# Kernel optimization log

Hardware: AMD Instinct MI355X
Metric: run time of the kernel (lower is better)

The kernel has to match this reference:

```python
import jax, jax.numpy as jnp
import numpy as np

B, C, H, W = 16, 512, 32, 32
COND_C, L_COND = 768, 77
N_GROUPS, N_HEADS = 8, 8
HEAD = C // N_HEADS
EPS = 1e-5


def setup_inputs() -> dict:
    key = jax.random.key(0)
    ks = jax.random.split(key, 6)
    s = lambda fan_in: 1.0 / np.sqrt(fan_in)
    return {
        "x_0": jax.random.normal(ks[0], (B, C, H, W), jnp.float32),
        "cond": jax.random.normal(ks[1], (B, L_COND, COND_C), jnp.float32),
        "gn_gamma": jnp.ones((C,), jnp.float32),
        "gn_beta": jnp.zeros((C,), jnp.float32),
        "qkv_w": jax.random.normal(ks[2], (3 * C, C), jnp.float32) * s(C),
        "qkv_b": jnp.zeros((3 * C,), jnp.float32),
        "cond_kv_w": jax.random.normal(ks[3], (2 * C, COND_C), jnp.float32) * s(COND_C),
        "cond_kv_b": jnp.zeros((2 * C,), jnp.float32),
        "out_w": jax.random.normal(ks[4], (C, C), jnp.float32) * s(C),
        "out_b": jnp.zeros((C,), jnp.float32),
    }


def reference(x_0, cond, gn_gamma, gn_beta, qkv_w, qkv_b, cond_kv_w, cond_kv_b, out_w, out_b):
    b, c, h, w = x_0.shape
    L = h * w
    # --- GroupNorm over (C/G, H, W) per group, per-channel affine ---
    xg = x_0.reshape(b, N_GROUPS, c // N_GROUPS, h * w)
    mu = xg.mean(axis=(2, 3), keepdims=True)
    var = xg.var(axis=(2, 3), keepdims=True)
    xn = ((xg - mu) * jax.lax.rsqrt(var + EPS)).reshape(b, c, h, w)
    xn = xn * gn_gamma[None, :, None, None] + gn_beta[None, :, None, None]
    # --- to tokens [B, L, C] ---
    x = xn.transpose(0, 2, 3, 1).reshape(b, L, c)
    # --- QKV ---
    qkv = x @ qkv_w.T + qkv_b  # [B, L, 3C]
    q, k, v = jnp.split(qkv, 3, axis=-1)
    q = q.reshape(b, L, N_HEADS, HEAD)
    k = k.reshape(b, L, N_HEADS, HEAD)
    v = v.reshape(b, L, N_HEADS, HEAD)
    # --- conditional K/V ---
    kv_c = cond @ cond_kv_w.T + cond_kv_b  # [B, Lc, 2C]
    k_c, v_c = jnp.split(kv_c, 2, axis=-1)
    Lc = cond.shape[1]
    k_c = k_c.reshape(b, Lc, N_HEADS, HEAD)
    v_c = v_c.reshape(b, Lc, N_HEADS, HEAD)
    K = jnp.concatenate([k, k_c], axis=1)  # [B, L+Lc, H, D]
    V = jnp.concatenate([v, v_c], axis=1)
    # --- attention (full score matrix, as in the original) ---
    scale = HEAD ** -0.5
    scores = jnp.einsum("bqhd,bkhd->bhqk", q, K) * scale
    att = jax.nn.softmax(scores, axis=-1)
    out = jnp.einsum("bhqk,bkhd->bqhd", att, V).reshape(b, L, c)
    out = out @ out_w.T + out_b
    # --- back to image + residual ---
    out = out.reshape(b, h, w, c).transpose(0, 3, 1, 2)
    return out + x_0
```

## Files before the change

### kernel.cpp

```cpp
#include <hip/hip_runtime.h>

typedef short bf16x8 __attribute__((ext_vector_type(8)));
typedef float f32x4 __attribute__((ext_vector_type(4)));
typedef float f32x16 __attribute__((ext_vector_type(16)));
typedef unsigned int u32x4 __attribute__((ext_vector_type(4)));

#define KVP 1152

__device__ __forceinline__ unsigned short f2b(float f) {
    unsigned int u = __float_as_uint(f);
    u += 0x7FFFu + ((u >> 16) & 1u);
    return (unsigned short)(u >> 16);
}

__device__ __forceinline__ f32x4 mfma16(bf16x8 a, bf16x8 b, f32x4 c) {
    return __builtin_amdgcn_mfma_f32_16x16x32_bf16(a, b, c, 0, 0, 0);
}
__device__ __forceinline__ f32x16 mfma32(bf16x8 a, bf16x8 b, f32x16 c) {
    return __builtin_amdgcn_mfma_f32_32x32x16_bf16(a, b, c, 0, 0, 0);
}
__device__ __forceinline__ float exp2_raw(float x) {
    float r; asm("v_exp_f32 %0, %1" : "=v"(r) : "v"(x)); return r;
}
__device__ __forceinline__ unsigned cvt_pk(float lo, float hi) {
    unsigned r; asm("v_cvt_pk_bf16_f32 %0, %1, %2" : "=v"(r) : "v"(lo), "v"(hi)); return r;
}

typedef __attribute__((address_space(3))) unsigned int lds_u32_t;
typedef const __attribute__((address_space(1))) unsigned int glb_u32_t;
__device__ __forceinline__ void async_cp16(const void* g, void* l) {
    __builtin_amdgcn_global_load_lds((glb_u32_t*)(unsigned long long)g,
                                     (lds_u32_t*)(unsigned int)(unsigned long long)l,
                                     16, 0, 0);
}

__global__ __launch_bounds__(256) void gn_stats_k(const float* __restrict__ x, float* __restrict__ stats) {
    int bg = blockIdx.x;
    const float4* p = (const float4*)(x + (size_t)bg * 64 * 1024);
    float s = 0.f, ss = 0.f;
    for (int i = threadIdx.x; i < 16384; i += 256) {
        float4 v = p[i];
        s  += v.x + v.y + v.z + v.w;
        ss += v.x * v.x + v.y * v.y + v.z * v.z + v.w * v.w;
    }
#pragma unroll
    for (int o = 32; o; o >>= 1) { s += __shfl_down(s, o); ss += __shfl_down(ss, o); }
    __shared__ float red[8];
    int w = threadIdx.x >> 6;
    if ((threadIdx.x & 63) == 0) { red[w] = s; red[4 + w] = ss; }
    __syncthreads();
    if (threadIdx.x == 0) {
        s  = red[0] + red[1] + red[2] + red[3];
        ss = red[4] + red[5] + red[6] + red[7];
        float mean = s * (1.f / 65536.f);
        float var  = ss * (1.f / 65536.f) - mean * mean;
        stats[2 * bg]     = mean;
        stats[2 * bg + 1] = rsqrtf(var + 1e-5f);
    }
}

__global__ __launch_bounds__(256) void gn_apply_k(const float* __restrict__ x, const float* __restrict__ stats,
                                                  const float* __restrict__ gamma, const float* __restrict__ beta,
                                                  unsigned short* __restrict__ xt) {
    int st = blockIdx.x & 15;
    int ct = (blockIdx.x >> 4) & 7;
    int b  = blockIdx.x >> 7;
    float mean = stats[2 * (b * 8 + ct)];
    float rsig = stats[2 * (b * 8 + ct) + 1];
    __shared__ unsigned short tile[64][65];
    int tid = threadIdx.x;
#pragma unroll
    for (int it = 0; it < 4; ++it) {
        int idx = it * 256 + tid;
        int ci = idx >> 4, j4 = idx & 15;
        int c = ct * 64 + ci;
        float4 v = *(const float4*)(x + ((size_t)b * 512 + c) * 1024 + st * 64 + j4 * 4);
        float gs = gamma[c] * rsig;
        float bo = beta[c] - mean * gs;
        tile[j4 * 4 + 0][ci] = f2b(v.x * gs + bo);
        tile[j4 * 4 + 1][ci] = f2b(v.y * gs + bo);
        tile[j4 * 4 + 2][ci] = f2b(v.z * gs + bo);
        tile[j4 * 4 + 3][ci] = f2b(v.w * gs + bo);
    }
    __syncthreads();
#pragma unroll
    for (int it = 0; it < 4; ++it) {
        int idx = it * 256 + tid;
        int si = idx >> 4, q = idx & 15;
        uint2 u;
        u.x = (unsigned)tile[si][q * 4 + 0] | ((unsigned)tile[si][q * 4 + 1] << 16);
        u.y = (unsigned)tile[si][q * 4 + 2] | ((unsigned)tile[si][q * 4 + 3] << 16);
        *(uint2*)(xt + ((size_t)b * 1024 + st * 64 + si) * 512 + ct * 64 + q * 4) = u;
    }
}

__global__ __launch_bounds__(256) void cvt_k(const float* __restrict__ in, unsigned short* __restrict__ out, int n4) {
    int i = blockIdx.x * 256 + threadIdx.x;
    if (i < n4) {
        float4 v = ((const float4*)in)[i];
        uint2 u;
        u.x = (unsigned)f2b(v.x) | ((unsigned)f2b(v.y) << 16);
        u.y = (unsigned)f2b(v.z) | ((unsigned)f2b(v.w) << 16);
        ((uint2*)out)[i] = u;
    }
}

template <int EPI>
__global__ __launch_bounds__(256) void gemm128_k(const unsigned short* __restrict__ A,
                                                 const unsigned short* __restrict__ Bw,
                                                 const float* __restrict__ bias,
                                                 int M, int N, int K,
                                                 unsigned short* __restrict__ Qo,
                                                 unsigned short* __restrict__ Ko,
                                                 unsigned short* __restrict__ Vo,
                                                 const float* __restrict__ x0,
                                                 float* __restrict__ outp) {
    __shared__ __align__(16) unsigned short As[3][4096];
    __shared__ __align__(16) unsigned short Bs[3][4096];
    const int m0 = blockIdx.x * 128, n0 = blockIdx.y * 128;
    const int tid = threadIdx.x, lane = tid & 63, w = tid >> 6;
    const int wr = w >> 1, wc = w & 1;
    const int lc = lane & 15, lg = lane >> 4;

    const int sRow = lane >> 2;
    const int sSlot = (lane & 3) ^ ((lane >> 3) & 3);
    const unsigned short* aSrc0 = A + (size_t)(m0 + 16 * w + sRow) * K + sSlot * 8;
    const unsigned short* aSrc1 = A + (size_t)(m0 + 64 + 16 * w + sRow) * K + sSlot * 8;
    const unsigned short* bSrc0 = Bw + (size_t)(n0 + 16 * w + sRow) * K + sSlot * 8;
    const unsigned short* bSrc1 = Bw + (size_t)(n0 + 64 + 16 * w + sRow) * K + sSlot * 8;

    const int rSlot8 = (lg ^ ((lc >> 1) & 3)) * 8;

    f32x4 acc[4][4];
#pragma unroll
    for (int m = 0; m < 4; ++m)
#pragma unroll
        for (int n = 0; n < 4; ++n) acc[m][n] = (f32x4){0.f, 0.f, 0.f, 0.f};

    const int nT = K >> 5;
    async_cp16(aSrc0, &As[0][w * 512]);
    async_cp16(aSrc1, &As[0][(4 + w) * 512]);
    async_cp16(bSrc0, &Bs[0][w * 512]);
    async_cp16(bSrc1, &Bs[0][(4 + w) * 512]);
    async_cp16(aSrc0 + 32, &As[1][w * 512]);
    async_cp16(aSrc1 + 32, &As[1][(4 + w) * 512]);
    async_cp16(bSrc0 + 32, &Bs[1][w * 512]);
    async_cp16(bSrc1 + 32, &Bs[1][(4 + w) * 512]);

    int c = 0;
#pragma unroll 1
    for (int t = 0; t < nT; ++t) {
        if (t + 2 < nT) {
            int c2 = c + 2; if (c2 >= 3) c2 -= 3;
            const int k2 = (t + 2) << 5;
            async_cp16(aSrc0 + k2, &As[c2][w * 512]);
            async_cp16(aSrc1 + k2, &As[c2][(4 + w) * 512]);
            async_cp16(bSrc0 + k2, &Bs[c2][w * 512]);
            async_cp16(bSrc1 + k2, &Bs[c2][(4 + w) * 512]);
            asm volatile("s_waitcnt vmcnt(8)" ::: "memory");
        } else if (t + 1 < nT) {
            asm volatile("s_waitcnt vmcnt(4)" ::: "memory");
        } else {
            asm volatile("s_waitcnt vmcnt(0)" ::: "memory");
        }
        __builtin_amdgcn_s_barrier();

        bf16x8 af[4], bfr[4];
#pragma unroll
        for (int m = 0; m < 4; ++m)
            af[m] = *(const bf16x8*)&As[c][(wr * 64 + m * 16 + lc) * 32 + rSlot8];
#pragma unroll
        for (int n = 0; n < 4; ++n)
            bfr[n] = *(const bf16x8*)&Bs[c][(wc * 64 + n * 16 + lc) * 32 + rSlot8];
        asm volatile("s_waitcnt lgkmcnt(0)" ::: "memory");
        __builtin_amdgcn_sched_barrier(0);
        __builtin_amdgcn_s_barrier();

#pragma unroll
        for (int m = 0; m < 4; ++m)
#pragma unroll
            for (int n = 0; n < 4; ++n)
                acc[m][n] = mfma16(af[m], bfr[n], acc[m][n]);

        ++c; if (c == 3) c = 0;
    }

#pragma unroll
    for (int n = 0; n < 4; ++n) {
        int col = n0 + wc * 64 + n * 16 + lc;
        float bv = bias[col];
#pragma unroll
        for (int m = 0; m < 4; ++m) {
            int rb = m0 + wr * 64 + m * 16 + lg * 4;
#pragma unroll
            for (int r = 0; r < 4; ++r) {
                int token = rb + r;
                float val = acc[m][n][r] + bv;
                if (EPI == 0) {
                    int b = token >> 10, l = token & 1023;
                    if (col < 512) {
                        int hh = col >> 6, d = col & 63;
                        Qo[((size_t)(b * 8 + hh) * 1024 + l) * 64 + d] = f2b(val * (0.125f * 1.44269504089f));
                    } else if (col < 1024) {
                        int j = col - 512, hh = j >> 6, d = j & 63;
                        Ko[((size_t)(b * 8 + hh) * KVP + l) * 64 + d] = f2b(val);
                    } else {
                        int j = col - 1024, hh = j >> 6, d = j & 63;
                        Vo[((size_t)(b * 8 + hh) * 64 + d) * KVP + l] = f2b(val);
                    }
                } else {
                    int b = token >> 10, hw = token & 1023;
                    size_t a = ((size_t)b * 512 + col) * 1024 + hw;
                    outp[a] = val + x0[a];
                }
            }
        }
    }
}

__global__ __launch_bounds__(256) void gemm_nt_k(const unsigned short* __restrict__ A,
                                                 const unsigned short* __restrict__ Bw,
                                                 const float* __restrict__ bias,
                                                 int M, int N, int K,
                                                 unsigned short* __restrict__ Ko,
                                                 unsigned short* __restrict__ Vo) {
    __shared__ unsigned short As[64][40];
    __shared__ unsigned short Bs[64][40];
    const int m0 = blockIdx.x * 64, n0 = blockIdx.y * 64;
    const int tid = threadIdx.x, lane = tid & 63, w = tid >> 6;
    const int lc = lane & 15, lg = lane >> 4;
    const int lrow = tid >> 2, lseg = tid & 3;
    f32x4 acc[4];
#pragma unroll
    for (int i = 0; i < 4; ++i) acc[i] = (f32x4){0.f, 0.f, 0.f, 0.f};

    for (int k0 = 0; k0 < K; k0 += 32) {
        uint4 av = make_uint4(0u, 0u, 0u, 0u);
        if (m0 + lrow < M) av = *(const uint4*)(A + (size_t)(m0 + lrow) * K + k0 + lseg * 8);
        *(uint4*)&As[lrow][lseg * 8] = av;
        uint4 bv = *(const uint4*)(Bw + (size_t)(n0 + lrow) * K + k0 + lseg * 8);
        *(uint4*)&Bs[lrow][lseg * 8] = bv;
        __syncthreads();
        bf16x8 af = *(const bf16x8*)&As[w * 16 + lc][lg * 8];
#pragma unroll
        for (int ct = 0; ct < 4; ++ct) {
            bf16x8 bfr = *(const bf16x8*)&Bs[ct * 16 + lc][lg * 8];
            acc[ct] = mfma16(af, bfr, acc[ct]);
        }
        __syncthreads();
    }

    const int rbase = m0 + w * 16 + lg * 4;
#pragma unroll
    for (int ct = 0; ct < 4; ++ct) {
        int col = n0 + ct * 16 + lc;
        float bv = bias[col];
#pragma unroll
        for (int r = 0; r < 4; ++r) {
            int token = rbase + r;
            if (token >= M) continue;
            float val = acc[ct][r] + bv;
            int b = token / 77, l = token - b * 77;
            if (col < 512) {
                int hh = col >> 6, d = col & 63;
                Ko[((size_t)(b * 8 + hh) * KVP + 1024 + l) * 64 + d] = f2b(val);
            } else {
                int j = col - 512, hh = j >> 6, d = j & 63;
                Vo[((size_t)(b * 8 + hh) * 64 + d) * KVP + 1024 + l] = f2b(val);
            }
        }
    }
}

__global__ __launch_bounds__(512) void attn2_k(const unsigned short* __restrict__ Q,
                                               const unsigned short* __restrict__ Kb,
                                               const unsigned short* __restrict__ Vt,
                                               unsigned short* __restrict__ atok) {
    __shared__ __align__(16) unsigned short lds[18432];

    const int bh = blockIdx.x >> 2;
    const int qt = blockIdx.x & 3;
    const int w  = threadIdx.x >> 6;
    const int lane = threadIdx.x & 63;
    const int ql = lane & 31, hi = lane >> 5;
    const int q0 = qt * 256 + w * 32;

    bf16x8 qf[4];
    const unsigned short* Qp = Q + ((size_t)bh * 1024 + q0 + ql) * 64 + hi * 8;
#pragma unroll
    for (int ks = 0; ks < 4; ++ks) qf[ks] = *(const bf16x8*)(Qp + ks * 16);

    const unsigned short* Kg = Kb + (size_t)bh * KVP * 64;
    const unsigned short* Vg = Vt + (size_t)bh * 64 * KVP;

    const int srow = lane >> 3;
    const int sc   = (((lane & 7) ^ (lane >> 3)) << 3);

    f32x16 o0, o1;
#pragma unroll
    for (int i = 0; i < 16; ++i) { o0[i] = 0.f; o1[i] = 0.f; }
    float mreg = -1e30f, lsum = 0.f;

    {
        uint4 kr = *(const uint4*)(Kg + (size_t)(8 * w + srow) * 64 + sc);
        uint4 vr = *(const uint4*)(Vg + (size_t)(8 * w + srow) * KVP + sc);
        *(uint4*)&lds[w * 512 + lane * 8] = kr;
        *(uint4*)&lds[4096 + w * 512 + lane * 8] = vr;
    }
    __syncthreads();

    int cur = 0;
    for (int it = 0; it < 18; ++it) {
        const int kv0 = it * 64;
        const bool pre = (it < 17);
        uint4 kn, vn;
        if (pre) {
            kn = *(const uint4*)(Kg + (size_t)(kv0 + 64 + 8 * w + srow) * 64 + sc);
            vn = *(const uint4*)(Vg + (size_t)(8 * w + srow) * KVP + kv0 + 64 + sc);
        }
        const int kb = cur * 8192, vb = cur * 8192 + 4096;

        f32x16 s0, s1;
#pragma unroll
        for (int i = 0; i < 16; ++i) { s0[i] = 0.f; s1[i] = 0.f; }
#pragma unroll
        for (int ks = 0; ks < 4; ++ks) {
            const int sl = ((ks * 2 + hi) ^ (ql & 7)) << 3;
            bf16x8 kf0 = *(const bf16x8*)&lds[kb + ql * 64 + sl];
            bf16x8 kf1 = *(const bf16x8*)&lds[kb + (32 + ql) * 64 + sl];
            s0 = mfma32(kf0, qf[ks], s0);
            s1 = mfma32(kf1, qf[ks], s1);
        }
        if (kv0 == 1088) {
#pragma unroll
            for (int r = 0; r < 16; ++r) {
                int kva = 1088 + (r & 3) + 8 * (r >> 2) + 4 * hi;
                if (kva >= 1101) s0[r] = -1e30f;
                if (kva + 32 >= 1101) s1[r] = -1e30f;
            }
        }

        float t[16];
#pragma unroll
        for (int i = 0; i < 16; ++i) t[i] = fmaxf(s0[i], s1[i]);
#pragma unroll
        for (int st = 8; st; st >>= 1)
#pragma unroll
            for (int i = 0; i < st; ++i) t[i] = fmaxf(t[i], t[i + st]);
        float pmax = fmaxf(t[0], __shfl_xor(t[0], 32));

        if (__any(pmax > mreg + 8.f)) {
            float mn = fmaxf(mreg, pmax);
            float al = exp2_raw(mreg - mn);
            mreg = mn;
            lsum *= al;
#pragma unroll
            for (int i = 0; i < 16; ++i) { o0[i] *= al; o1[i] *= al; }
        }

        unsigned pk0[8], pk1[8];
        float sA = 0.f, sB = 0.f, sC = 0.f, sD = 0.f;
#pragma unroll
        for (int i = 0; i < 8; ++i) {
            float a0 = exp2_raw(s0[2 * i] - mreg), a1 = exp2_raw(s0[2 * i + 1] - mreg);
            float b0 = exp2_raw(s1[2 * i] - mreg), b1 = exp2_raw(s1[2 * i + 1] - mreg);
            pk0[i] = cvt_pk(a0, a1);
            pk1[i] = cvt_pk(b0, b1);
            sA += a0; sB += a1; sC += b0; sD += b1;
        }
        float ls = (sA + sB) + (sC + sD);
        ls += __shfl_xor(ls, 32);
        lsum += ls;

#pragma unroll
        for (int t2 = 0; t2 < 2; ++t2) {
            const unsigned* pk = t2 ? pk1 : pk0;
#pragma unroll
            for (int v = 0; v < 2; ++v) {
                unsigned a0 = pk[4 * v], a1 = pk[4 * v + 1], a2 = pk[4 * v + 2], a3 = pk[4 * v + 3];
                unsigned x = __shfl_xor(hi ? a0 : a2, 32);
                unsigned y = __shfl_xor(hi ? a1 : a3, 32);
                u32x4 fw;
                fw.x = hi ? x : a0; fw.y = hi ? y : a1; fw.z = hi ? a2 : x; fw.w = hi ? a3 : y;
                bf16x8 pf = __builtin_bit_cast(bf16x8, fw);
                const int ks2 = 2 * t2 + v;
                const int sl = ((ks2 * 2 + hi) ^ (ql & 7)) << 3;
                bf16x8 vf0 = *(const bf16x8*)&lds[vb + ql * 64 + sl];
                bf16x8 vf1 = *(const bf16x8*)&lds[vb + (32 + ql) * 64 + sl];
                o0 = mfma32(vf0, pf, o0);
                o1 = mfma32(vf1, pf, o1);
            }
        }

        if (pre) {
            *(uint4*)&lds[(cur ^ 1) * 8192 + w * 512 + lane * 8] = kn;
            *(uint4*)&lds[(cur ^ 1) * 8192 + 4096 + w * 512 + lane * 8] = vn;
        }
        __syncthreads();
        cur ^= 1;
    }

    float rinv = 1.f / lsum;
    unsigned short* sw = &lds[w * 2304];
#pragma unroll
    for (int dt = 0; dt < 2; ++dt) {
#pragma unroll
        for (int rp = 0; rp < 8; ++rp) {
            float e0 = (dt ? o1[2 * rp] : o0[2 * rp]) * rinv;
            float e1 = (dt ? o1[2 * rp + 1] : o0[2 * rp + 1]) * rinv;
            int d = dt * 32 + ((2 * rp) & 3) + 8 * ((2 * rp) >> 2) + 4 * hi;
            *(unsigned*)&sw[ql * 72 + d] = cvt_pk(e0, e1);
        }
    }
    __syncthreads();
    {
        int i = threadIdx.x >> 1, hf = threadIdx.x & 1;
        const unsigned short* src = &lds[(i >> 5) * 2304 + (i & 31) * 72 + hf * 32];
        u32x4 r0 = *(const u32x4*)(src);
        u32x4 r1 = *(const u32x4*)(src + 8);
        u32x4 r2 = *(const u32x4*)(src + 16);
        u32x4 r3 = *(const u32x4*)(src + 24);
        int b = bh >> 3, h = bh & 7;
        unsigned short* gd = atok + ((size_t)b * 1024 + qt * 256 + i) * 512 + h * 64 + hf * 32;
        *(u32x4*)(gd) = r0;
        *(u32x4*)(gd + 8) = r1;
        *(u32x4*)(gd + 16) = r2;
        *(u32x4*)(gd + 24) = r3;
    }
}

extern "C" void kernel_launch(void* const* d_in, const int* in_sizes, int n_in,
                              void* d_out, int out_size, void* d_ws, size_t ws_size,
                              hipStream_t stream) {
    const float* x0     = (const float*)d_in[0];
    const float* cond   = (const float*)d_in[1];
    const float* gamma  = (const float*)d_in[2];
    const float* beta   = (const float*)d_in[3];
    const float* qkv_w  = (const float*)d_in[4];
    const float* qkv_b  = (const float*)d_in[5];
    const float* ckv_w  = (const float*)d_in[6];
    const float* ckv_b  = (const float*)d_in[7];
    const float* out_w  = (const float*)d_in[8];
    const float* out_b  = (const float*)d_in[9];
    float* outp = (float*)d_out;

    char* p = (char*)d_ws;
    float* stats = (float*)p;            p += 1024;
    unsigned short* xt    = (unsigned short*)p; p += (size_t)16384 * 512 * 2;
    unsigned short* wqkv  = (unsigned short*)p; p += (size_t)1536 * 512 * 2;
    unsigned short* wckv  = (unsigned short*)p; p += (size_t)1024 * 768 * 2;
    unsigned short* wout  = (unsigned short*)p; p += (size_t)512 * 512 * 2;
    unsigned short* condb = (unsigned short*)p; p += (size_t)1232 * 768 * 2;
    unsigned short* Qb    = (unsigned short*)p; p += (size_t)16 * 8 * 1024 * 64 * 2;
    unsigned short* Kb    = (unsigned short*)p; p += (size_t)16 * 8 * KVP * 64 * 2;
    unsigned short* Vtb   = (unsigned short*)p; p += (size_t)16 * 8 * KVP * 64 * 2;
    unsigned short* atok  = (unsigned short*)p; p += (size_t)16384 * 512 * 2;

    gn_stats_k<<<128, 256, 0, stream>>>(x0, stats);
    gn_apply_k<<<2048, 256, 0, stream>>>(x0, stats, gamma, beta, xt);
    cvt_k<<<768, 256, 0, stream>>>(qkv_w, wqkv, 196608);
    cvt_k<<<768, 256, 0, stream>>>(ckv_w, wckv, 196608);
    cvt_k<<<256, 256, 0, stream>>>(out_w, wout, 65536);
    cvt_k<<<924, 256, 0, stream>>>(cond, condb, 236544);

    gemm128_k<0><<<dim3(128, 12), 256, 0, stream>>>(xt, wqkv, qkv_b, 16384, 1536, 512,
                                                    Qb, Kb, Vtb, nullptr, nullptr);
    gemm_nt_k<<<dim3(20, 16), 256, 0, stream>>>(condb, wckv, ckv_b, 1232, 1024, 768, Kb, Vtb);
    attn2_k<<<512, 512, 0, stream>>>(Qb, Kb, Vtb, atok);
    gemm128_k<2><<<dim3(128, 4), 256, 0, stream>>>(atok, wout, out_b, 16384, 512, 512,
                                                   nullptr, nullptr, nullptr, x0, outp);
}
```

Baseline: 187.8 us.

## Vectorize GEMM epilogues via operand swap and split GroupNorm stats into partials

The GroupNorm stats kernel now launches 512 blocks that each write a partial sum and sum of squares, and the apply kernel combines the four partials per group. This raises parallelism over 128 long-running blocks. The QKV GEMM is split into a Q/K launch, which swaps MFMA operands so each lane holds four consecutive channels and can store packed 8-byte bf16 writes, and a separate V launch that stores four consecutive tokens into the transposed V layout. The output GEMM epilogue now uses float4 loads and stores for the residual. The aim is fewer, wider global stores instead of scattered 2-byte and 4-byte accesses, at the cost of one extra kernel launch.

```diff
diff --git a/kernel.cpp b/kernel.cpp
--- a/kernel.cpp
+++ b/kernel.cpp
@@ -34,11 +34,11 @@
                                      16, 0, 0);
 }
 
-__global__ __launch_bounds__(256) void gn_stats_k(const float* __restrict__ x, float* __restrict__ stats) {
-    int bg = blockIdx.x;
-    const float4* p = (const float4*)(x + (size_t)bg * 64 * 1024);
+__global__ __launch_bounds__(256) void gn_part_k(const float* __restrict__ x, float2* __restrict__ part) {
+    int blk = blockIdx.x;
+    const float4* p = (const float4*)(x + (size_t)blk * 16384);
     float s = 0.f, ss = 0.f;
-    for (int i = threadIdx.x; i < 16384; i += 256) {
+    for (int i = threadIdx.x; i < 4096; i += 256) {
         float4 v = p[i];
         s  += v.x + v.y + v.z + v.w;
         ss += v.x * v.x + v.y * v.y + v.z * v.z + v.w * v.w;
@@ -52,21 +52,23 @@
     if (threadIdx.x == 0) {
         s  = red[0] + red[1] + red[2] + red[3];
         ss = red[4] + red[5] + red[6] + red[7];
-        float mean = s * (1.f / 65536.f);
-        float var  = ss * (1.f / 65536.f) - mean * mean;
-        stats[2 * bg]     = mean;
-        stats[2 * bg + 1] = rsqrtf(var + 1e-5f);
-    }
-}
-
-__global__ __launch_bounds__(256) void gn_apply_k(const float* __restrict__ x, const float* __restrict__ stats,
+        part[blk] = make_float2(s, ss);
+    }
+}
+
+__global__ __launch_bounds__(256) void gn_apply_k(const float* __restrict__ x, const float2* __restrict__ part,
                                                   const float* __restrict__ gamma, const float* __restrict__ beta,
                                                   unsigned short* __restrict__ xt) {
     int st = blockIdx.x & 15;
     int ct = (blockIdx.x >> 4) & 7;
     int b  = blockIdx.x >> 7;
-    float mean = stats[2 * (b * 8 + ct)];
-    float rsig = stats[2 * (b * 8 + ct) + 1];
+    int bg = b * 8 + ct;
+    float2 p0 = part[4 * bg], p1 = part[4 * bg + 1], p2 = part[4 * bg + 2], p3 = part[4 * bg + 3];
+    float s = (p0.x + p1.x) + (p2.x + p3.x);
+    float ss = (p0.y + p1.y) + (p2.y + p3.y);
+    float mean = s * (1.f / 65536.f);
+    float var  = ss * (1.f / 65536.f) - mean * mean;
+    float rsig = rsqrtf(var + 1e-5f);
     __shared__ unsigned short tile[64][65];
     int tid = threadIdx.x;
 #pragma unroll
@@ -109,7 +111,7 @@
 __global__ __launch_bounds__(256) void gemm128_k(const unsigned short* __restrict__ A,
                                                  const unsigned short* __restrict__ Bw,
                                                  const float* __restrict__ bias,
-                                                 int M, int N, int K,
+                                                 int K,
                                                  unsigned short* __restrict__ Qo,
                                                  unsigned short* __restrict__ Ko,
                                                  unsigned short* __restrict__ Vo,
@@ -179,40 +181,70 @@
 #pragma unroll
         for (int m = 0; m < 4; ++m)
 #pragma unroll
-            for (int n = 0; n < 4; ++n)
-                acc[m][n] = mfma16(af[m], bfr[n], acc[m][n]);
+            for (int n = 0; n < 4; ++n) {
+                if (EPI == 0) acc[m][n] = mfma16(bfr[n], af[m], acc[m][n]);
+                else          acc[m][n] = mfma16(af[m], bfr[n], acc[m][n]);
+            }
 
         ++c; if (c == 3) c = 0;
     }
 
-#pragma unroll
-    for (int n = 0; n < 4; ++n) {
-        int col = n0 + wc * 64 + n * 16 + lc;
-        float bv = bias[col];
-#pragma unroll
-        for (int m = 0; m < 4; ++m) {
-            int rb = m0 + wr * 64 + m * 16 + lg * 4;
-#pragma unroll
-            for (int r = 0; r < 4; ++r) {
-                int token = rb + r;
-                float val = acc[m][n][r] + bv;
-                if (EPI == 0) {
-                    int b = token >> 10, l = token & 1023;
-                    if (col < 512) {
-                        int hh = col >> 6, d = col & 63;
-                        Qo[((size_t)(b * 8 + hh) * 1024 + l) * 64 + d] = f2b(val * (0.125f * 1.44269504089f));
-                    } else if (col < 1024) {
-                        int j = col - 512, hh = j >> 6, d = j & 63;
-                        Ko[((size_t)(b * 8 + hh) * KVP + l) * 64 + d] = f2b(val);
-                    } else {
-                        int j = col - 1024, hh = j >> 6, d = j & 63;
-                        Vo[((size_t)(b * 8 + hh) * 64 + d) * KVP + l] = f2b(val);
-                    }
+    if (EPI == 0) {
+        const bool isQ = (n0 < 512);
+        const float sc = isQ ? (0.125f * 1.44269504089f) : 1.f;
+#pragma unroll
+        for (int n = 0; n < 4; ++n) {
+            const int c0 = n0 + wc * 64 + n * 16 + lg * 4;
+            const float4 b4 = *(const float4*)&bias[c0];
+#pragma unroll
+            for (int m = 0; m < 4; ++m) {
+                const int tok = m0 + wr * 64 + m * 16 + lc;
+                const int b = tok >> 10, l = tok & 1023;
+                float v0 = (acc[m][n][0] + b4.x) * sc;
+                float v1 = (acc[m][n][1] + b4.y) * sc;
+                float v2 = (acc[m][n][2] + b4.z) * sc;
+                float v3 = (acc[m][n][3] + b4.w) * sc;
+                uint2 u = make_uint2(cvt_pk(v0, v1), cvt_pk(v2, v3));
+                if (isQ) {
+                    const int hh = c0 >> 6, d = c0 & 63;
+                    *(uint2*)(Qo + ((size_t)(b * 8 + hh) * 1024 + l) * 64 + d) = u;
                 } else {
-                    int b = token >> 10, hw = token & 1023;
-                    size_t a = ((size_t)b * 512 + col) * 1024 + hw;
-                    outp[a] = val + x0[a];
+                    const int hh = (c0 - 512) >> 6, d = c0 & 63;
+                    *(uint2*)(Ko + ((size_t)(b * 8 + hh) * KVP + l) * 64 + d) = u;
                 }
+            }
+        }
+    } else if (EPI == 1) {
+#pragma unroll
+        for (int n = 0; n < 4; ++n) {
+            const int j = n0 + wc * 64 + n * 16 + lc;
+            const int hh = j >> 6, d = j & 63;
+            const float bv = bias[j];
+#pragma unroll
+            for (int m = 0; m < 4; ++m) {
+                const int t0 = m0 + wr * 64 + m * 16 + lg * 4;
+                const int b = t0 >> 10, l0 = t0 & 1023;
+                uint2 u = make_uint2(cvt_pk(acc[m][n][0] + bv, acc[m][n][1] + bv),
+                                     cvt_pk(acc[m][n][2] + bv, acc[m][n][3] + bv));
+                *(uint2*)(Vo + ((size_t)(b * 8 + hh) * 64 + d) * KVP + l0) = u;
+            }
+        }
+    } else {
+#pragma unroll
+        for (int n = 0; n < 4; ++n) {
+            const int col = n0 + wc * 64 + n * 16 + lc;
+            const float bv = bias[col];
+#pragma unroll
+            for (int m = 0; m < 4; ++m) {
+                const int t0 = m0 + wr * 64 + m * 16 + lg * 4;
+                const size_t a = ((size_t)(t0 >> 10) * 512 + col) * 1024 + (t0 & 1023);
+                float4 xv = *(const float4*)(x0 + a);
+                float4 o;
+                o.x = acc[m][n][0] + bv + xv.x;
+                o.y = acc[m][n][1] + bv + xv.y;
+                o.z = acc[m][n][2] + bv + xv.z;
+                o.w = acc[m][n][3] + bv + xv.w;
+                *(float4*)(outp + a) = o;
             }
         }
     }
@@ -445,7 +477,7 @@
     float* outp = (float*)d_out;
 
     char* p = (char*)d_ws;
-    float* stats = (float*)p;            p += 1024;
+    float2* part = (float2*)p;           p += 4096;
     unsigned short* xt    = (unsigned short*)p; p += (size_t)16384 * 512 * 2;
     unsigned short* wqkv  = (unsigned short*)p; p += (size_t)1536 * 512 * 2;
     unsigned short* wckv  = (unsigned short*)p; p += (size_t)1024 * 768 * 2;
@@ -456,17 +488,19 @@
     unsigned short* Vtb   = (unsigned short*)p; p += (size_t)16 * 8 * KVP * 64 * 2;
     unsigned short* atok  = (unsigned short*)p; p += (size_t)16384 * 512 * 2;
 
-    gn_stats_k<<<128, 256, 0, stream>>>(x0, stats);
-    gn_apply_k<<<2048, 256, 0, stream>>>(x0, stats, gamma, beta, xt);
+    gn_part_k<<<512, 256, 0, stream>>>(x0, part);
+    gn_apply_k<<<2048, 256, 0, stream>>>(x0, part, gamma, beta, xt);
     cvt_k<<<768, 256, 0, stream>>>(qkv_w, wqkv, 196608);
     cvt_k<<<768, 256, 0, stream>>>(ckv_w, wckv, 196608);
     cvt_k<<<256, 256, 0, stream>>>(out_w, wout, 65536);
     cvt_k<<<924, 256, 0, stream>>>(cond, condb, 236544);
 
-    gemm128_k<0><<<dim3(128, 12), 256, 0, stream>>>(xt, wqkv, qkv_b, 16384, 1536, 512,
-                                                    Qb, Kb, Vtb, nullptr, nullptr);
+    gemm128_k<0><<<dim3(128, 8), 256, 0, stream>>>(xt, wqkv, qkv_b, 512,
+                                                   Qb, Kb, nullptr, nullptr, nullptr);
+    gemm128_k<1><<<dim3(128, 4), 256, 0, stream>>>(xt, wqkv + (size_t)1024 * 512, qkv_b + 1024, 512,
+                                                   nullptr, nullptr, Vtb, nullptr, nullptr);
     gemm_nt_k<<<dim3(20, 16), 256, 0, stream>>>(condb, wckv, ckv_b, 1232, 1024, 768, Kb, Vtb);
     attn2_k<<<512, 512, 0, stream>>>(Qb, Kb, Vtb, atok);
-    gemm128_k<2><<<dim3(128, 4), 256, 0, stream>>>(atok, wout, out_b, 16384, 512, 512,
+    gemm128_k<2><<<dim3(128, 4), 256, 0, stream>>>(atok, wout, out_b, 512,
                                                    nullptr, nullptr, nullptr, x0, outp);
 }
```

After: 179.7 us. 4.3% less time.
